# Kernel optimization log

Hardware: AMD Instinct MI355X
Metric: run time of the kernel (lower is better)

## Reference

```python
import jax, jax.numpy as jnp
import numpy as np

SIZE_IN = (8, 8, 8, 8)
SIZE_OUT = (8, 8, 8, 8)
RANK = (1, 16, 16, 16, 1)
BATCH = 8192


def setup_inputs() -> dict:
    key = jax.random.key(0)
    ks = jax.random.split(key, 6)
    inp = {"x": jax.random.normal(ks[0], (BATCH,) + SIZE_IN, jnp.float32)}
    for k in range(4):
        # TT-matrix core: [r_{k-1}, n_out_k, n_in_k, r_k]
        c = jax.random.normal(ks[k + 1], (RANK[k], SIZE_OUT[k], SIZE_IN[k], RANK[k + 1]), jnp.float32) * 0.1
        inp[f"core{k}"] = c
    inp["bias"] = jax.random.normal(ks[5], SIZE_OUT, jnp.float32) * 0.01
    return inp


def tt_dense_matvec(cores, x):
    # y[b, n1..nd] = sum_{m1..md, r0..rd} prod_k core_k[r_{k-1}, n_k, m_k, r_k] * x[b, m1..md]
    d = len(cores)
    Ms = [c.shape[2] for c in cores]
    Ns = [c.shape[1] for c in cores]
    batch = x.shape[:-d]
    B = int(np.prod(batch)) if batch else 1
    # running tensor shape: [L, r_k, M_{k+1}..Md flattened], L = B * N1..Nk
    T = x.reshape(B, 1, -1)  # [B, r0=1, M1*..*Md]
    for k, c in enumerate(cores):
        r0, n, m, r1 = c.shape
        rest = int(np.prod(Ms[k + 1:])) if k + 1 < d else 1
        Tm = T.reshape(-1, r0 * m, rest)                      # [L, r0*m, rest]
        Cm = c.transpose(0, 2, 1, 3).reshape(r0 * m, n * r1)  # [r0*m, n*r1]
        T = jnp.einsum('lpr,pq->lqr', Tm, Cm)                 # [L, n*r1, rest]
        T = T.reshape(-1, r1, rest)                           # fold n into L
    return T.reshape(batch + tuple(Ns))


def reference(x, core0, core1, core2, core3, bias):
    return tt_dense_matvec([core0, core1, core2, core3], x) + bias
```

## Files before the change

### kernel.cpp

```cpp
#include <hip/hip_runtime.h>


typedef __attribute__((ext_vector_type(8))) short bf16x8;
typedef __attribute__((ext_vector_type(4))) float f32x4;

__device__ __forceinline__ short f2bf(float f) {
    union { float f; unsigned u; } v; v.f = f;
    unsigned u = v.u;
    u += 0x7fffu + ((u >> 16) & 1u);
    return (short)(u >> 16);
}

__global__ void tt_pre(const float* __restrict__ c0, const float* __restrict__ c1,
                       const float* __restrict__ c2, const float* __restrict__ c3,
                       short* __restrict__ ws) {
    int id = blockIdx.x * 256 + threadIdx.x;
    if (id < 65536) {
        int p  = id & 63, q = (id >> 6) & 127, n1 = id >> 13;
        int m1 = p >> 3, m2 = p & 7, n2 = q >> 4, r2 = q & 15;
        float s = 0.f;
        #pragma unroll
        for (int r1 = 0; r1 < 16; ++r1)
            s += c0[(n1 * 8 + m1) * 16 + r1] * c1[((r1 * 8 + n2) * 8 + m2) * 16 + r2];
        ws[id] = f2bf(s);
    } else {
        int id2 = id - 65536;
        int s_  = id2 & 1023, row = id2 >> 10;
        int n3 = row >> 3, n4 = row & 7;
        int m3 = s_ >> 7, m4 = (s_ >> 4) & 7, r2s = s_ & 15;
        int r2 = (r2s - 4 * (m3 & 1)) & 15;
        float s = 0.f;
        #pragma unroll
        for (int r3 = 0; r3 < 16; ++r3)
            s += c2[((r2 * 8 + n3) * 8 + m3) * 16 + r3] * c3[(r3 * 8 + n4) * 8 + m4];
        ws[65536 + id2] = f2bf(s);
    }
}

#define XT_S 72
#define T2_S 1032
#define BUFSH (16 * T2_S)

__global__ __launch_bounds__(256, 2) void tt_main(
    const float* __restrict__ x, const short* __restrict__ ws,
    const float* __restrict__ bias, float* __restrict__ out)
{
    __shared__ short lds2[2 * BUFSH];

    const short* cc  = ws;
    const short* c23 = ws + 65536;

    const int t = threadIdx.x, w = t >> 6, L = t & 63;
    const int quad = L >> 4, l16 = L & 15;
    const long long b0 = (long long)blockIdx.x * 2;
    const int mh = w >> 1, nh = w & 1;

    short* xt = lds2 + BUFSH;

    {
        const float* xb = x + (b0 + (w >> 1)) * 4096;
        const int pr = (w & 1) * 32;
        short* dst = &xt[(((w >> 1) * 64 + L) * XT_S) + pr];
        #pragma unroll
        for (int g = 0; g < 4; ++g) {
            bf16x8 v;
            #pragma unroll
            for (int j = 0; j < 8; ++j) v[j] = f2bf(xb[(pr + g * 8 + j) * 64 + L]);
            *(bf16x8*)(dst + g * 8) = v;
        }
    }

    bf16x8 a2[32];
    {
        const short* base = c23 + (16 * w + l16) * 1024 + quad * 8;
        #pragma unroll
        for (int kt = 0; kt < 32; ++kt) a2[kt] = *(const bf16x8*)(base + kt * 32);
    }

    bf16x8 a1pf[4];
    auto pfload = [&](int n1) {
        const short* ab = cc + n1 * 8192 + (mh * 64 + l16) * 64 + quad * 8;
        a1pf[0] = *(const bf16x8*)(ab);
        a1pf[1] = *(const bf16x8*)(ab + 1024);
        a1pf[2] = *(const bf16x8*)(ab + 32);
        a1pf[3] = *(const bf16x8*)(ab + 1024 + 32);
    };
    pfload(0);

    __syncthreads();

    bf16x8 b01[8];
    #pragma unroll
    for (int kt = 0; kt < 2; ++kt)
        #pragma unroll
        for (int nt = 0; nt < 4; ++nt)
            b01[kt * 4 + nt] =
                *(const bf16x8*)&xt[(nh * 64 + nt * 16 + l16) * XT_S + kt * 32 + quad * 8];

    __syncthreads();

    auto stage01 = [&](int n1, short* dst) {
        #pragma unroll
        for (int h = 0; h < 2; ++h) {
            bf16x8 a1[4];
            if (h == 0) {
                a1[0] = a1pf[0]; a1[1] = a1pf[1]; a1[2] = a1pf[2]; a1[3] = a1pf[3];
            } else {
                const short* ab = cc + n1 * 8192 + (mh * 64 + 32 + l16) * 64 + quad * 8;
                a1[0] = *(const bf16x8*)(ab);
                a1[1] = *(const bf16x8*)(ab + 1024);
                a1[2] = *(const bf16x8*)(ab + 32);
                a1[3] = *(const bf16x8*)(ab + 1024 + 32);
            }
            f32x4 acc[2][4] = {};
            #pragma unroll
            for (int mt2 = 0; mt2 < 2; ++mt2)
                #pragma unroll
                for (int nt = 0; nt < 4; ++nt) {
                    acc[mt2][nt] = __builtin_amdgcn_mfma_f32_16x16x32_bf16(
                        a1[mt2], b01[nt], acc[mt2][nt], 0, 0, 0);
                    acc[mt2][nt] = __builtin_amdgcn_mfma_f32_16x16x32_bf16(
                        a1[2 + mt2], b01[4 + nt], acc[mt2][nt], 0, 0, 0);
                }
            #pragma unroll
            for (int mt2 = 0; mt2 < 2; ++mt2) {
                const int n2 = mh * 4 + h * 2 + mt2;
                #pragma unroll
                for (int nt = 0; nt < 4; ++nt) {
                    const int u  = nt * 16 + l16;
                    const int m3 = u >> 3, m4 = u & 7;
                    const int rblk = (quad * 4 + 4 * (m3 & 1)) & 15;
                    int2 pk;
                    pk.x = (int)((unsigned short)f2bf(acc[mt2][nt][0]) |
                                 ((unsigned)(unsigned short)f2bf(acc[mt2][nt][1]) << 16));
                    pk.y = (int)((unsigned short)f2bf(acc[mt2][nt][2]) |
                                 ((unsigned)(unsigned short)f2bf(acc[mt2][nt][3]) << 16));
                    *(int2*)&dst[(nh * 8 + n2) * T2_S + (m3 * 8 + m4) * 16 + rblk] = pk;
                }
            }
        }
    };

    stage01(0, lds2);
    __syncthreads();

    #pragma unroll 1
    for (int k = 0; k < 8; ++k) {
        if (k < 7) pfload(k + 1);

        f32x4 d0 = {}, d1 = {}, d2 = {}, d3 = {};
        {
            const short* tb = &lds2[(k & 1) * BUFSH + l16 * T2_S + quad * 8];
            __builtin_amdgcn_s_setprio(1);
            #pragma unroll
            for (int kt = 0; kt < 32; kt += 4) {
                bf16x8 f0 = *(const bf16x8*)(tb + kt * 32);
                bf16x8 f1 = *(const bf16x8*)(tb + kt * 32 + 32);
                bf16x8 f2 = *(const bf16x8*)(tb + kt * 32 + 64);
                bf16x8 f3 = *(const bf16x8*)(tb + kt * 32 + 96);
                d0 = __builtin_amdgcn_mfma_f32_16x16x32_bf16(a2[kt],     f0, d0, 0, 0, 0);
                d1 = __builtin_amdgcn_mfma_f32_16x16x32_bf16(a2[kt + 1], f1, d1, 0, 0, 0);
                d2 = __builtin_amdgcn_mfma_f32_16x16x32_bf16(a2[kt + 2], f2, d2, 0, 0, 0);
                d3 = __builtin_amdgcn_mfma_f32_16x16x32_bf16(a2[kt + 3], f3, d3, 0, 0, 0);
            }
            __builtin_amdgcn_s_setprio(0);
        }
        {
            const int bp = l16 >> 3, n2 = l16 & 7;
            const int off = k * 512 + n2 * 64 + 16 * w + quad * 4;
            const float4 bv = *(const float4*)(bias + off);
            float4 ov;
            ov.x = d0[0] + d1[0] + d2[0] + d3[0] + bv.x;
            ov.y = d0[1] + d1[1] + d2[1] + d3[1] + bv.y;
            ov.z = d0[2] + d1[2] + d2[2] + d3[2] + bv.z;
            ov.w = d0[3] + d1[3] + d2[3] + d3[3] + bv.w;
            *(float4*)(out + (b0 + bp) * 4096 + off) = ov;
        }

        if (k < 7) {
            stage01(k + 1, lds2 + ((k + 1) & 1) * BUFSH);
            __syncthreads();
        }
    }
}

extern "C" void kernel_launch(void* const* d_in, const int* in_sizes, int n_in,
                              void* d_out, int out_size, void* d_ws, size_t ws_size,
                              hipStream_t stream) {
    const float* x    = (const float*)d_in[0];
    const float* c0   = (const float*)d_in[1];
    const float* c1   = (const float*)d_in[2];
    const float* c2   = (const float*)d_in[3];
    const float* c3   = (const float*)d_in[4];
    const float* bias = (const float*)d_in[5];
    float* out = (float*)d_out;
    short* ws  = (short*)d_ws;

    hipLaunchKernelGGL(tt_pre, dim3(512), dim3(256), 0, stream, c0, c1, c2, c3, ws);
    hipLaunchKernelGGL(tt_main, dim3(4096), dim3(256), 0, stream, x, ws, bias, out);
}
```

Before: 415.7 us.

## Split stage-2 K dimension across waves with LDS partial-sum reduction, single buffer

Each wave now reads only its own quarter of the staged T2 tile and multiplies it against all four output row-tiles, instead of reading the whole tile for a single output tile. Partial sums are exchanged through a new fp32 LDS scratch array and reduced by the owning wave. The T2 buffer goes from double- to single-buffered, which cuts LDS reads per wave but adds a barrier and LDS write/read traffic for the reduction. Without the double buffer, stage01 for the next n1 can no longer overlap with reads of the current tile.

Result: no change. 423.6 us (+1.9%).

```diff
diff --git a/kernel.cpp b/kernel.cpp
--- a/kernel.cpp
+++ b/kernel.cpp
@@ -39,13 +39,13 @@
 
 #define XT_S 72
 #define T2_S 1032
-#define BUFSH (16 * T2_S)
 
 __global__ __launch_bounds__(256, 2) void tt_main(
     const float* __restrict__ x, const short* __restrict__ ws,
     const float* __restrict__ bias, float* __restrict__ out)
 {
-    __shared__ short lds2[2 * BUFSH];
+    __shared__ short t2t[16 * T2_S];
+    __shared__ float psum[3072];
 
     const short* cc  = ws;
     const short* c23 = ws + 65536;
@@ -55,7 +55,7 @@
     const long long b0 = (long long)blockIdx.x * 2;
     const int mh = w >> 1, nh = w & 1;
 
-    short* xt = lds2 + BUFSH;
+    short* xt = t2t;
 
     {
         const float* xb = x + (b0 + (w >> 1)) * 4096;
@@ -72,9 +72,12 @@
 
     bf16x8 a2[32];
     {
-        const short* base = c23 + (16 * w + l16) * 1024 + quad * 8;
-        #pragma unroll
-        for (int kt = 0; kt < 32; ++kt) a2[kt] = *(const bf16x8*)(base + kt * 32);
+        const short* base = c23 + l16 * 1024 + w * 256 + quad * 8;
+        #pragma unroll
+        for (int rt = 0; rt < 4; ++rt)
+            #pragma unroll
+            for (int kt = 0; kt < 8; ++kt)
+                a2[rt * 8 + kt] = *(const bf16x8*)(base + rt * 16 * 1024 + kt * 32);
     }
 
     bf16x8 a1pf[4];
@@ -99,7 +102,7 @@
 
     __syncthreads();
 
-    auto stage01 = [&](int n1, short* dst) {
+    auto stage01 = [&](int n1) {
         #pragma unroll
         for (int h = 0; h < 2; ++h) {
             bf16x8 a1[4];
@@ -135,50 +138,68 @@
                                  ((unsigned)(unsigned short)f2bf(acc[mt2][nt][1]) << 16));
                     pk.y = (int)((unsigned short)f2bf(acc[mt2][nt][2]) |
                                  ((unsigned)(unsigned short)f2bf(acc[mt2][nt][3]) << 16));
-                    *(int2*)&dst[(nh * 8 + n2) * T2_S + (m3 * 8 + m4) * 16 + rblk] = pk;
+                    *(int2*)&t2t[(nh * 8 + n2) * T2_S + (m3 * 8 + m4) * 16 + rblk] = pk;
                 }
             }
         }
     };
 
-    stage01(0, lds2);
+    stage01(0);
     __syncthreads();
 
     #pragma unroll 1
     for (int k = 0; k < 8; ++k) {
         if (k < 7) pfload(k + 1);
 
-        f32x4 d0 = {}, d1 = {}, d2 = {}, d3 = {};
+        f32x4 d[4] = {};
+        f32x4 down;
         {
-            const short* tb = &lds2[(k & 1) * BUFSH + l16 * T2_S + quad * 8];
+            const short* tb = &t2t[l16 * T2_S + w * 256 + quad * 8];
             __builtin_amdgcn_s_setprio(1);
             #pragma unroll
-            for (int kt = 0; kt < 32; kt += 4) {
-                bf16x8 f0 = *(const bf16x8*)(tb + kt * 32);
-                bf16x8 f1 = *(const bf16x8*)(tb + kt * 32 + 32);
-                bf16x8 f2 = *(const bf16x8*)(tb + kt * 32 + 64);
-                bf16x8 f3 = *(const bf16x8*)(tb + kt * 32 + 96);
-                d0 = __builtin_amdgcn_mfma_f32_16x16x32_bf16(a2[kt],     f0, d0, 0, 0, 0);
-                d1 = __builtin_amdgcn_mfma_f32_16x16x32_bf16(a2[kt + 1], f1, d1, 0, 0, 0);
-                d2 = __builtin_amdgcn_mfma_f32_16x16x32_bf16(a2[kt + 2], f2, d2, 0, 0, 0);
-                d3 = __builtin_amdgcn_mfma_f32_16x16x32_bf16(a2[kt + 3], f3, d3, 0, 0, 0);
+            for (int kt = 0; kt < 8; ++kt) {
+                bf16x8 bf = *(const bf16x8*)(tb + kt * 32);
+                #pragma unroll
+                for (int rt = 0; rt < 4; ++rt)
+                    d[rt] = __builtin_amdgcn_mfma_f32_16x16x32_bf16(
+                        a2[rt * 8 + kt], bf, d[rt], 0, 0, 0);
             }
             __builtin_amdgcn_s_setprio(0);
         }
+        #pragma unroll
+        for (int rt = 0; rt < 4; ++rt) {
+            if (rt == w) {
+                down = d[rt];
+            } else {
+                const int s = rt - (rt > w ? 1 : 0);
+                *(f32x4*)&psum[((w * 3 + s) * 64 + L) * 4] = d[rt];
+            }
+        }
+        __syncthreads();
+
         {
+            #pragma unroll
+            for (int w2 = 0; w2 < 4; ++w2) {
+                if (w2 != w) {
+                    const int s = w - (w > w2 ? 1 : 0);
+                    f32x4 p = *(const f32x4*)&psum[((w2 * 3 + s) * 64 + L) * 4];
+                    down[0] += p[0]; down[1] += p[1];
+                    down[2] += p[2]; down[3] += p[3];
+                }
+            }
             const int bp = l16 >> 3, n2 = l16 & 7;
             const int off = k * 512 + n2 * 64 + 16 * w + quad * 4;
             const float4 bv = *(const float4*)(bias + off);
             float4 ov;
-            ov.x = d0[0] + d1[0] + d2[0] + d3[0] + bv.x;
-            ov.y = d0[1] + d1[1] + d2[1] + d3[1] + bv.y;
-            ov.z = d0[2] + d1[2] + d2[2] + d3[2] + bv.z;
-            ov.w = d0[3] + d1[3] + d2[3] + d3[3] + bv.w;
+            ov.x = down[0] + bv.x;
+            ov.y = down[1] + bv.y;
+            ov.z = down[2] + bv.z;
+            ov.w = down[3] + bv.w;
             *(float4*)(out + (b0 + bp) * 4096 + off) = ov;
         }
 
         if (k < 7) {
-            stage01(k + 1, lds2 + ((k + 1) & 1) * BUFSH);
+            stage01(k + 1);
             __syncthreads();
         }
     }
```

## Split stage-2/3 K dimension across wave pairs with LDS partial-sum exchange

Applied to the files above, without the earlier changes.

Stage 2 is re-partitioned so each wave loads 32 rows of the combined core23 matrix but only half of the K range. Each LDS B fragment is now reused by two MFMAs, which halves the LDS reads per wave. Partial sums are swapped between wave pairs through a small shared buffer, and this exchange is placed before the next stage01 and its barrier so it shares one sync per iteration. Float-to-bf16 packing also switches to the packed __float22bfloat162_rn intrinsic. The cost is extra LDS and an extra cross-wave dependency.

Measured after the change: 410.6 us. About the same (-1.2%).

```diff
diff --git a/kernel.cpp b/kernel.cpp
--- a/kernel.cpp
+++ b/kernel.cpp
@@ -1,4 +1,5 @@
 #include <hip/hip_runtime.h>
+#include <hip/hip_bf16.h>
 
 
 typedef __attribute__((ext_vector_type(8))) short bf16x8;
@@ -9,6 +10,12 @@
     unsigned u = v.u;
     u += 0x7fffu + ((u >> 16) & 1u);
     return (short)(u >> 16);
+}
+
+__device__ __forceinline__ int pk2bf(float lo, float hi) {
+    union { __hip_bfloat162 h; int i; } u;
+    u.h = __float22bfloat162_rn(make_float2(lo, hi));
+    return u.i;
 }
 
 __global__ void tt_pre(const float* __restrict__ c0, const float* __restrict__ c1,
@@ -45,7 +52,8 @@
     const float* __restrict__ x, const short* __restrict__ ws,
     const float* __restrict__ bias, float* __restrict__ out)
 {
-    __shared__ short lds2[2 * BUFSH];
+    __shared__ short t2t[2 * BUFSH];
+    __shared__ float psum[2][1024];
 
     const short* cc  = ws;
     const short* c23 = ws + 65536;
@@ -53,33 +61,39 @@
     const int t = threadIdx.x, w = t >> 6, L = t & 63;
     const int quad = L >> 4, l16 = L & 15;
     const long long b0 = (long long)blockIdx.x * 2;
-    const int mh = w >> 1, nh = w & 1;
-
-    short* xt = lds2 + BUFSH;
+    const int rh = w >> 1, kh = w & 1;
+
+    short* xt = t2t;
 
     {
-        const float* xb = x + (b0 + (w >> 1)) * 4096;
-        const int pr = (w & 1) * 32;
-        short* dst = &xt[(((w >> 1) * 64 + L) * XT_S) + pr];
+        const float* xb = x + (b0 + rh) * 4096;
+        const int pr = kh * 32;
+        short* dst = &xt[((rh * 64 + L) * XT_S) + pr];
         #pragma unroll
         for (int g = 0; g < 4; ++g) {
-            bf16x8 v;
-            #pragma unroll
-            for (int j = 0; j < 8; ++j) v[j] = f2bf(xb[(pr + g * 8 + j) * 64 + L]);
-            *(bf16x8*)(dst + g * 8) = v;
+            float f[8];
+            #pragma unroll
+            for (int j = 0; j < 8; ++j) f[j] = xb[(pr + g * 8 + j) * 64 + L];
+            int4 pk;
+            pk.x = pk2bf(f[0], f[1]); pk.y = pk2bf(f[2], f[3]);
+            pk.z = pk2bf(f[4], f[5]); pk.w = pk2bf(f[6], f[7]);
+            *(int4*)(dst + g * 8) = pk;
         }
     }
 
     bf16x8 a2[32];
     {
-        const short* base = c23 + (16 * w + l16) * 1024 + quad * 8;
-        #pragma unroll
-        for (int kt = 0; kt < 32; ++kt) a2[kt] = *(const bf16x8*)(base + kt * 32);
+        const short* base = c23 + (32 * rh + l16) * 1024 + 512 * kh + quad * 8;
+        #pragma unroll
+        for (int rt = 0; rt < 2; ++rt)
+            #pragma unroll
+            for (int kt = 0; kt < 16; ++kt)
+                a2[rt * 16 + kt] = *(const bf16x8*)(base + rt * 16 * 1024 + kt * 32);
     }
 
     bf16x8 a1pf[4];
     auto pfload = [&](int n1) {
-        const short* ab = cc + n1 * 8192 + (mh * 64 + l16) * 64 + quad * 8;
+        const short* ab = cc + n1 * 8192 + (rh * 64 + l16) * 64 + quad * 8;
         a1pf[0] = *(const bf16x8*)(ab);
         a1pf[1] = *(const bf16x8*)(ab + 1024);
         a1pf[2] = *(const bf16x8*)(ab + 32);
@@ -95,18 +109,18 @@
         #pragma unroll
         for (int nt = 0; nt < 4; ++nt)
             b01[kt * 4 + nt] =
-                *(const bf16x8*)&xt[(nh * 64 + nt * 16 + l16) * XT_S + kt * 32 + quad * 8];
+                *(const bf16x8*)&xt[(kh * 64 + nt * 16 + l16) * XT_S + kt * 32 + quad * 8];
 
     __syncthreads();
 
-    auto stage01 = [&](int n1, short* dst) {
+    auto stage01 = [&](int n1, short* dstbuf) {
         #pragma unroll
         for (int h = 0; h < 2; ++h) {
             bf16x8 a1[4];
             if (h == 0) {
                 a1[0] = a1pf[0]; a1[1] = a1pf[1]; a1[2] = a1pf[2]; a1[3] = a1pf[3];
             } else {
-                const short* ab = cc + n1 * 8192 + (mh * 64 + 32 + l16) * 64 + quad * 8;
+                const short* ab = cc + n1 * 8192 + (rh * 64 + 32 + l16) * 64 + quad * 8;
                 a1[0] = *(const bf16x8*)(ab);
                 a1[1] = *(const bf16x8*)(ab + 1024);
                 a1[2] = *(const bf16x8*)(ab + 32);
@@ -124,62 +138,70 @@
                 }
             #pragma unroll
             for (int mt2 = 0; mt2 < 2; ++mt2) {
-                const int n2 = mh * 4 + h * 2 + mt2;
+                const int n2 = rh * 4 + h * 2 + mt2;
                 #pragma unroll
                 for (int nt = 0; nt < 4; ++nt) {
                     const int u  = nt * 16 + l16;
                     const int m3 = u >> 3, m4 = u & 7;
                     const int rblk = (quad * 4 + 4 * (m3 & 1)) & 15;
                     int2 pk;
-                    pk.x = (int)((unsigned short)f2bf(acc[mt2][nt][0]) |
-                                 ((unsigned)(unsigned short)f2bf(acc[mt2][nt][1]) << 16));
-                    pk.y = (int)((unsigned short)f2bf(acc[mt2][nt][2]) |
-                                 ((unsigned)(unsigned short)f2bf(acc[mt2][nt][3]) << 16));
-                    *(int2*)&dst[(nh * 8 + n2) * T2_S + (m3 * 8 + m4) * 16 + rblk] = pk;
+                    pk.x = pk2bf(acc[mt2][nt][0], acc[mt2][nt][1]);
+                    pk.y = pk2bf(acc[mt2][nt][2], acc[mt2][nt][3]);
+                    *(int2*)&dstbuf[(kh * 8 + n2) * T2_S + (m3 * 8 + m4) * 16 + rblk] = pk;
                 }
             }
         }
     };
 
-    stage01(0, lds2);
+    stage01(0, t2t);
     __syncthreads();
 
     #pragma unroll 1
     for (int k = 0; k < 8; ++k) {
+        const int p = k & 1;
         if (k < 7) pfload(k + 1);
 
-        f32x4 d0 = {}, d1 = {}, d2 = {}, d3 = {};
+        f32x4 d2[4] = {};
         {
-            const short* tb = &lds2[(k & 1) * BUFSH + l16 * T2_S + quad * 8];
+            const short* tb = &t2t[p * BUFSH + l16 * T2_S + kh * 512 + quad * 8];
             __builtin_amdgcn_s_setprio(1);
             #pragma unroll
-            for (int kt = 0; kt < 32; kt += 4) {
-                bf16x8 f0 = *(const bf16x8*)(tb + kt * 32);
-                bf16x8 f1 = *(const bf16x8*)(tb + kt * 32 + 32);
-                bf16x8 f2 = *(const bf16x8*)(tb + kt * 32 + 64);
-                bf16x8 f3 = *(const bf16x8*)(tb + kt * 32 + 96);
-                d0 = __builtin_amdgcn_mfma_f32_16x16x32_bf16(a2[kt],     f0, d0, 0, 0, 0);
-                d1 = __builtin_amdgcn_mfma_f32_16x16x32_bf16(a2[kt + 1], f1, d1, 0, 0, 0);
-                d2 = __builtin_amdgcn_mfma_f32_16x16x32_bf16(a2[kt + 2], f2, d2, 0, 0, 0);
-                d3 = __builtin_amdgcn_mfma_f32_16x16x32_bf16(a2[kt + 3], f3, d3, 0, 0, 0);
+            for (int kt = 0; kt < 16; kt += 2) {
+                bf16x8 bf0 = *(const bf16x8*)(tb + kt * 32);
+                bf16x8 bf1 = *(const bf16x8*)(tb + kt * 32 + 32);
+                d2[0] = __builtin_amdgcn_mfma_f32_16x16x32_bf16(a2[kt],          bf0, d2[0], 0, 0, 0);
+                d2[1] = __builtin_amdgcn_mfma_f32_16x16x32_bf16(a2[kt + 1],      bf1, d2[1], 0, 0, 0);
+                d2[2] = __builtin_amdgcn_mfma_f32_16x16x32_bf16(a2[16 + kt],     bf0, d2[2], 0, 0, 0);
+                d2[3] = __builtin_amdgcn_mfma_f32_16x16x32_bf16(a2[16 + kt + 1], bf1, d2[3], 0, 0, 0);
             }
             __builtin_amdgcn_s_setprio(0);
         }
+        f32x4 down, dfor;
         {
+            f32x4 dt0, dt1;
+            #pragma unroll
+            for (int i = 0; i < 4; ++i) { dt0[i] = d2[0][i] + d2[1][i];
+                                          dt1[i] = d2[2][i] + d2[3][i]; }
+            if (kh == 0) { down = dt0; dfor = dt1; }
+            else         { down = dt1; dfor = dt0; }
+        }
+        *(f32x4*)&psum[p][(rh * 2 + (1 - kh)) * 256 + L * 4] = dfor;
+
+        if (k < 7) stage01(k + 1, t2t + ((k + 1) & 1) * BUFSH);
+
+        __syncthreads();
+
+        {
+            f32x4 pp = *(const f32x4*)&psum[p][(rh * 2 + kh) * 256 + L * 4];
             const int bp = l16 >> 3, n2 = l16 & 7;
             const int off = k * 512 + n2 * 64 + 16 * w + quad * 4;
             const float4 bv = *(const float4*)(bias + off);
             float4 ov;
-            ov.x = d0[0] + d1[0] + d2[0] + d3[0] + bv.x;
-            ov.y = d0[1] + d1[1] + d2[1] + d3[1] + bv.y;
-            ov.z = d0[2] + d1[2] + d2[2] + d3[2] + bv.z;
-            ov.w = d0[3] + d1[3] + d2[3] + d3[3] + bv.w;
+            ov.x = down[0] + pp[0] + bv.x;
+            ov.y = down[1] + pp[1] + bv.y;
+            ov.z = down[2] + pp[2] + bv.z;
+            ov.w = down[3] + pp[3] + bv.w;
             *(float4*)(out + (b0 + bp) * 4096 + off) = ov;
-        }
-
-        if (k < 7) {
-            stage01(k + 1, lds2 + ((k + 1) & 1) * BUFSH);
-            __syncthreads();
         }
     }
 }
```
